# Optimization experiments

Hardware: AMD Instinct MI355X
Metric: run time of the kernel (lower is better)

Reference implementation:

```python
import jax, jax.numpy as jnp
import numpy as np

CHEB_K = 2  # chebyshev polynomial order (support_ks = [I, A] for cheb_k=2)


def _fc(x, w1, b1, w2, b2, w3, b3):
    # FC module: Linear -> sigmoid -> Linear -> sigmoid -> Linear
    h = jax.nn.sigmoid(x @ w1 + b1)
    h = jax.nn.sigmoid(h @ w2 + b2)
    return h @ w3 + b3


def _preprocess(adj):
    # adj: [B,N,N]; add self-loops then row-normalize
    adj = adj + jnp.eye(adj.shape[-1], dtype=adj.dtype)
    return adj / adj.sum(-1, keepdims=True)


def _gcn(x, adjs, ne, wpool, bpool):
    # x: [B,N,C], adjs: list of [B,N,N], ne: [N,E]
    # wpool: [E, 2*CHEB_K, C, O], bpool: [E, O]
    mats = []
    for A in adjs:
        ks = [jnp.broadcast_to(jnp.eye(A.shape[-1], dtype=A.dtype), A.shape), A]
        for _ in range(2, CHEB_K):
            ks.append(2.0 * jnp.matmul(A, ks[-1]) - ks[-2])
        mats.extend(ks)
    # [B,N,K,C] with K = 2*CHEB_K
    x_g = jnp.stack([jnp.einsum('bnm,bmc->bnc', S, x) for S in mats], axis=2)
    weights = jnp.einsum('nd,dkio->nkio', ne, wpool)  # [N,K,C,O]
    bias = ne @ bpool  # [N,O]
    return jnp.einsum('bnki,nkio->bno', x_g, weights) + bias


def _forward(x, state, ne0, ne1, ne2, fc1_w1, fc1_b1, fc1_w2, fc1_b2, fc1_w3, fc1_b3,
             fc2_w1, fc2_b1, fc2_w2, fc2_b2, fc2_w3, fc2_b3, gate_w, gate_b, upd_w, upd_b):
    hid = upd_w.shape[-1]
    ins = jnp.concatenate([x, state], axis=-1)  # [B,N,dim_in+hid]
    f1 = _fc(ins, fc1_w1, fc1_b1, fc1_w2, fc1_b2, fc1_w3, fc1_b3)  # [B,N,TD]
    f2 = _fc(ins, fc2_w1, fc2_b1, fc2_w2, fc2_b2, fc2_w3, fc2_b3)
    nv1 = jnp.tanh(ne0[:, None, :] * f1)  # einsum 'bd,bnd->bnd' == broadcast mul
    nv2 = jnp.tanh(ne1[:, None, :] * f2)
    adj = jnp.einsum('bnd,bmd->bnm', nv1, nv2) - jnp.einsum('bnd,bmd->bnm', nv2, nv1)
    adj1 = _preprocess(jax.nn.relu(adj))
    adj2 = _preprocess(jax.nn.relu(-jnp.swapaxes(adj, -2, -1)))
    z_r = jax.nn.sigmoid(_gcn(ins, [adj1, adj2], ne2, gate_w, gate_b))
    z, r = z_r[..., :hid], z_r[..., hid:]
    cand = jnp.concatenate([x, z * state], axis=-1)
    hc = jnp.tanh(_gcn(cand, [adj1, adj2], ne2, upd_w, upd_b))
    return r * state + (1.0 - r) * hc


def setup_inputs():
    B, N, DIN, DOUT, ED, TD = 32, 1024, 2, 64, 10, 32
    HG, MID = 16, 2  # hyperGNN_dim, middle_dim hardcoded in FC
    CIN = DIN + DOUT
    K2 = 2 * CHEB_K
    ks = jax.random.split(jax.random.key(0), 16)
    rn = lambda i, shape, s=1.0: jax.random.normal(ks[i], shape, dtype=jnp.float32) * s
    return {
        'x': rn(0, (B, N, DIN)),
        'state': rn(1, (B, N, DOUT)),
        'ne0': rn(2, (B, TD)),
        'ne1': rn(3, (B, TD)),
        'ne2': rn(4, (N, ED), 0.1),
        'fc1_w1': rn(5, (CIN, HG), 0.1), 'fc1_b1': jnp.zeros((HG,), jnp.float32),
        'fc1_w2': rn(6, (HG, MID), 0.1), 'fc1_b2': jnp.zeros((MID,), jnp.float32),
        'fc1_w3': rn(7, (MID, TD), 0.1), 'fc1_b3': jnp.zeros((TD,), jnp.float32),
        'fc2_w1': rn(8, (CIN, HG), 0.1), 'fc2_b1': jnp.zeros((HG,), jnp.float32),
        'fc2_w2': rn(9, (HG, MID), 0.1), 'fc2_b2': jnp.zeros((MID,), jnp.float32),
        'fc2_w3': rn(10, (MID, TD), 0.1), 'fc2_b3': jnp.zeros((TD,), jnp.float32),
        'gate_w': rn(11, (ED, K2, CIN, 2 * DOUT), 0.1),
        'gate_b': rn(12, (ED, 2 * DOUT), 0.1),
        'upd_w': rn(13, (ED, K2, CIN, DOUT), 0.1),
        'upd_b': rn(14, (ED, DOUT), 0.1),
    }


def reference(x, state, ne0, ne1, ne2, fc1_w1, fc1_b1, fc1_w2, fc1_b2, fc1_w3, fc1_b3,
              fc2_w1, fc2_b1, fc2_w2, fc2_b2, fc2_w3, fc2_b3, gate_w, gate_b, upd_w, upd_b):
    return _forward(x, state, ne0, ne1, ne2, fc1_w1, fc1_b1, fc1_w2, fc1_b2, fc1_w3, fc1_b3,
                    fc2_w1, fc2_b1, fc2_w2, fc2_b2, fc2_w3, fc2_b3, gate_w, gate_b, upd_w, upd_b)
```

## Files before the change

### kernel.cpp

```cpp
#include <hip/hip_runtime.h>
#include <math.h>

#define BB   32
#define NN   1024
#define DIN  2
#define DOUT 64
#define CIN  66
#define TD   32
#define ED   10
#define OG   128
#define OU   64
#define KP   160
#define XTR  80
#define PS   88

typedef __bf16 bf16x8 __attribute__((ext_vector_type(8)));
typedef float  f32x4  __attribute__((ext_vector_type(4)));
typedef short  s16x8  __attribute__((ext_vector_type(8)));

__device__ __forceinline__ unsigned short f2b(float f) {
    __bf16 h = (__bf16)f;
    return *(unsigned short*)&h;
}

__global__ __launch_bounds__(256) void k_pre(
    const float* __restrict__ x, const float* __restrict__ state,
    const float* __restrict__ ne0, const float* __restrict__ ne1,
    const float* __restrict__ ne2,
    const float* __restrict__ w11, const float* __restrict__ b11,
    const float* __restrict__ w12, const float* __restrict__ b12,
    const float* __restrict__ w13, const float* __restrict__ b13,
    const float* __restrict__ w21, const float* __restrict__ b21,
    const float* __restrict__ w22, const float* __restrict__ b22,
    const float* __restrict__ w23, const float* __restrict__ b23,
    const float* __restrict__ gate_w, const float* __restrict__ gate_b,
    const float* __restrict__ upd_w, const float* __restrict__ upd_b,
    unsigned short* __restrict__ nv1b, unsigned short* __restrict__ nv2b,
    unsigned short* __restrict__ XT0, unsigned short* __restrict__ XT1,
    unsigned short* __restrict__ BcTg, unsigned short* __restrict__ BcTu,
    float* __restrict__ biasG, float* __restrict__ biasU)
{
    __shared__ float sw[2408];
    __shared__ unsigned short st[68*72];
    int blk = blockIdx.x;
    int t = threadIdx.x;

    if (blk < 128) {
        const int oW1 = 0, oB1 = 1056, oW2 = 1072, oB2 = 1104, oW3 = 1108, oB3 = 1172, F2 = 1204;
        for (int i = t; i < 1056; i += 256) { sw[oW1+i] = w11[i]; sw[F2+oW1+i] = w21[i]; }
        if (t < 16) { sw[oB1+t] = b11[t]; sw[F2+oB1+t] = b21[t]; }
        if (t < 32) { sw[oW2+t] = w12[t]; sw[F2+oW2+t] = w22[t]; }
        if (t < 2)  { sw[oB2+t] = b12[t]; sw[F2+oB2+t] = b22[t]; }
        if (t < 64) { sw[oW3+t] = w13[t]; sw[F2+oW3+t] = w23[t]; }
        if (t >= 64 && t < 96) { sw[oB3+t-64] = b13[t-64]; sw[F2+oB3+t-64] = b23[t-64]; }
        __syncthreads();

        int p = blk*256 + t;
        int b = p >> 10;

        float h1a[16], h1b[16];
        #pragma unroll
        for (int j = 0; j < 16; ++j) { h1a[j] = sw[oB1+j]; h1b[j] = sw[F2+oB1+j]; }
        for (int i = 0; i < CIN; ++i) {
            float v = (i < DIN) ? x[(size_t)p*DIN + i] : state[(size_t)p*DOUT + (i-DIN)];
            #pragma unroll
            for (int jq = 0; jq < 4; ++jq) {
                float4 wa = *(const float4*)&sw[oW1 + i*16 + jq*4];
                float4 wb = *(const float4*)&sw[F2 + oW1 + i*16 + jq*4];
                h1a[jq*4+0] += v*wa.x; h1a[jq*4+1] += v*wa.y;
                h1a[jq*4+2] += v*wa.z; h1a[jq*4+3] += v*wa.w;
                h1b[jq*4+0] += v*wb.x; h1b[jq*4+1] += v*wb.y;
                h1b[jq*4+2] += v*wb.z; h1b[jq*4+3] += v*wb.w;
            }
        }
        #pragma unroll
        for (int j = 0; j < 16; ++j) {
            h1a[j] = 1.f/(1.f + __expf(-h1a[j]));
            h1b[j] = 1.f/(1.f + __expf(-h1b[j]));
        }
        float h2a0 = sw[oB2+0], h2a1 = sw[oB2+1];
        float h2b0 = sw[F2+oB2+0], h2b1 = sw[F2+oB2+1];
        #pragma unroll
        for (int i = 0; i < 16; ++i) {
            h2a0 += h1a[i]*sw[oW2 + i*2 + 0];
            h2a1 += h1a[i]*sw[oW2 + i*2 + 1];
            h2b0 += h1b[i]*sw[F2+oW2 + i*2 + 0];
            h2b1 += h1b[i]*sw[F2+oW2 + i*2 + 1];
        }
        h2a0 = 1.f/(1.f + __expf(-h2a0)); h2a1 = 1.f/(1.f + __expf(-h2a1));
        h2b0 = 1.f/(1.f + __expf(-h2b0)); h2b1 = 1.f/(1.f + __expf(-h2b1));

        const float* pn0 = ne0 + b*TD;
        const float* pn1 = ne1 + b*TD;
        #pragma unroll
        for (int jq = 0; jq < 8; ++jq) {
            float4 ba  = *(const float4*)&sw[oB3 + jq*4];
            float4 wa0 = *(const float4*)&sw[oW3 + jq*4];
            float4 wa1 = *(const float4*)&sw[oW3 + 32 + jq*4];
            float4 bb2 = *(const float4*)&sw[F2+oB3 + jq*4];
            float4 wb0 = *(const float4*)&sw[F2+oW3 + jq*4];
            float4 wb1 = *(const float4*)&sw[F2+oW3 + 32 + jq*4];
            float4 n0 = *(const float4*)&pn0[jq*4];
            float4 n1 = *(const float4*)&pn1[jq*4];
            ushort4 u1, u2;
            u1.x = f2b(tanhf(n0.x*(ba.x + h2a0*wa0.x + h2a1*wa1.x)));
            u1.y = f2b(tanhf(n0.y*(ba.y + h2a0*wa0.y + h2a1*wa1.y)));
            u1.z = f2b(tanhf(n0.z*(ba.z + h2a0*wa0.z + h2a1*wa1.z)));
            u1.w = f2b(tanhf(n0.w*(ba.w + h2a0*wa0.w + h2a1*wa1.w)));
            u2.x = f2b(tanhf(n1.x*(bb2.x + h2b0*wb0.x + h2b1*wb1.x)));
            u2.y = f2b(tanhf(n1.y*(bb2.y + h2b0*wb0.y + h2b1*wb1.y)));
            u2.z = f2b(tanhf(n1.z*(bb2.z + h2b0*wb0.z + h2b1*wb1.z)));
            u2.w = f2b(tanhf(n1.w*(bb2.w + h2b0*wb0.w + h2b1*wb1.w)));
            *(ushort4*)&nv1b[(size_t)p*TD + jq*4] = u1;
            *(ushort4*)&nv2b[(size_t)p*TD + jq*4] = u2;
        }
    } else if (blk < 640) {
        int idx = blk - 128;
        int b = idx >> 4, m0 = (idx & 15)*64;
        for (int i = t; i < 1024; i += 256) {
            int m = i >> 4, cq = i & 15;
            size_t base = (size_t)b*NN + m0 + m;
            float4 v = *(const float4*)&state[base*DOUT + cq*4];
            st[(2 + cq*4 + 0)*72 + m] = f2b(v.x);
            st[(2 + cq*4 + 1)*72 + m] = f2b(v.y);
            st[(2 + cq*4 + 2)*72 + m] = f2b(v.z);
            st[(2 + cq*4 + 3)*72 + m] = f2b(v.w);
        }
        if (t < 128) {
            int m = t >> 1, c = t & 1;
            st[c*72 + m] = f2b(x[((size_t)b*NN + m0 + m)*DIN + c]);
        }
        __syncthreads();
        const unsigned int ONE2 = 0x3F803F80u;
        for (int i = t; i < XTR*8; i += 256) {
            int c = i >> 3, ch = i & 7;
            uint4 v;
            if (c < 66)      v = *(const uint4*)&st[c*72 + ch*8];
            else if (c == 66) v = make_uint4(ONE2, ONE2, ONE2, ONE2);
            else              v = make_uint4(0, 0, 0, 0);
            *(uint4*)&XT0[((size_t)b*XTR + c)*NN + m0 + ch*8] = v;
            if (c < 2 || c >= 66)
                *(uint4*)&XT1[((size_t)b*XTR + c)*NN + m0 + ch*8] = v;
        }
    } else if (blk < 1840) {
        int tid = (blk - 640)*256 + t;
        int c = tid / KP, k = tid - c*KP;
        const float* pool; int O, cc; unsigned short* dst;
        if (c < 1280) { pool = gate_w; O = OG; cc = c;        dst = BcTg; }
        else          { pool = upd_w;  O = OU; cc = c - 1280; dst = BcTu; }
        int d = cc / O, o = cc - d*O;
        float v = 0.f;
        if (k < 132) {
            int kp = (k < 66) ? 0 : 1;
            int i  = (k < 66) ? k : k - 66;
            v = pool[(size_t)((d*4 + kp)*CIN + i)*O + o]
              + pool[(size_t)((d*4 + kp + 2)*CIN + i)*O + o];
        }
        dst[(size_t)cc*KP + k] = f2b(v);
    } else {
        int i = (blk - 1840)*256 + t;
        int n = i / 192, j = i - n*192;
        float v = 0.f;
        if (j < 128) {
            #pragma unroll
            for (int d = 0; d < ED; ++d) v += ne2[(size_t)n*ED + d]*gate_b[d*OG + j];
            biasG[(size_t)n*OG + j] = v;
        } else {
            int o = j - 128;
            #pragma unroll
            for (int d = 0; d < ED; ++d) v += ne2[(size_t)n*ED + d]*upd_b[d*OU + o];
            biasU[(size_t)n*OU + o] = v;
        }
    }
}

__global__ __launch_bounds__(512) void k_aapply(
    const unsigned short* __restrict__ nv1b, const unsigned short* __restrict__ nv2b,
    const unsigned short* __restrict__ XTg, unsigned short* __restrict__ A)
{
    __shared__ unsigned short s_nv1r[64*40], s_nv2r[64*40];
    __shared__ unsigned short s_nv1c[64*40], s_nv2c[64*40];
    __shared__ unsigned short s_p[64*PS];
    __shared__ unsigned short s_xt[80*72];
    __shared__ float s_rs[64];

    int t = threadIdx.x;
    int id = blockIdx.x;
    int b = id & 31, rbase = (id >> 5)*64;
    int w = t >> 6, lane = t & 63, lq = lane >> 4, ln = lane & 15;
    int g = w >> 1, sub = w & 1;

    {
        int arr = t >> 8, j = t & 255;
        int node = j >> 2, ch = j & 3;
        const unsigned short* src = (arr ? nv2b : nv1b)
            + ((size_t)b*NN + rbase + node)*TD + ch*8;
        unsigned short* dst = (arr ? s_nv2r : s_nv1r) + node*40 + ch*8;
        *(uint4*)dst = *(const uint4*)src;
    }
    __syncthreads();

    bf16x8 a1 = *(const bf16x8*)&s_nv1r[(16*g + ln)*40 + lq*8];
    s16x8 a2s = *(const s16x8*)&s_nv2r[(16*g + ln)*40 + lq*8];
    const s16x8 sgn = {(short)0x8000,(short)0x8000,(short)0x8000,(short)0x8000,
                       (short)0x8000,(short)0x8000,(short)0x8000,(short)0x8000};
    a2s ^= sgn;
    bf16x8 a2n = (bf16x8)a2s;

    f32x4 acc[3];
    #pragma unroll
    for (int i = 0; i < 3; ++i) acc[i] = (f32x4){0.f,0.f,0.f,0.f};
    const f32x4 zero4 = {0.f,0.f,0.f,0.f};

    for (int mb = 0; mb < NN; mb += 64) {
        __syncthreads();
        {
            int arr = t >> 8, j = t & 255;
            int node = j >> 2, ch = j & 3;
            const unsigned short* src = (arr ? nv2b : nv1b)
                + ((size_t)b*NN + mb + node)*TD + ch*8;
            unsigned short* dst = (arr ? s_nv2c : s_nv1c) + node*40 + ch*8;
            *(uint4*)dst = *(const uint4*)src;
        }
        for (int i = t; i < 640; i += 512) {
            int c = i >> 3, ch = i & 7;
            *(uint4*)&s_xt[c*72 + ch*8] =
                *(const uint4*)&XTg[((size_t)b*XTR + c)*NN + mb + ch*8];
        }
        __syncthreads();

        #pragma unroll
        for (int jj = 0; jj < 2; ++jj) {
            int j0 = (sub*2 + jj)*16;
            bf16x8 b2 = *(const bf16x8*)&s_nv2c[(j0 + ln)*40 + lq*8];
            bf16x8 b1 = *(const bf16x8*)&s_nv1c[(j0 + ln)*40 + lq*8];
            f32x4 s = __builtin_amdgcn_mfma_f32_16x16x32_bf16(a1,  b2, zero4, 0, 0, 0);
            s       = __builtin_amdgcn_mfma_f32_16x16x32_bf16(a2n, b1, s,     0, 0, 0);
            #pragma unroll
            for (int r = 0; r < 4; ++r) {
                float p = fmaxf(s[r], 0.f);
                *(__bf16*)&s_p[(16*g + lq*4 + r)*PS + j0 + ln] = (__bf16)p;
            }
        }
        __syncthreads();

        bf16x8 pa0 = *(const bf16x8*)&s_p[(16*g + ln)*PS +      lq*8];
        bf16x8 pa1 = *(const bf16x8*)&s_p[(16*g + ln)*PS + 32 + lq*8];
        if (sub == 0) {
            #pragma unroll
            for (int k = 0; k < 3; ++k) {
                int n0 = k*16;
                bf16x8 xb0 = *(const bf16x8*)&s_xt[(n0 + ln)*72 +      lq*8];
                bf16x8 xb1 = *(const bf16x8*)&s_xt[(n0 + ln)*72 + 32 + lq*8];
                acc[k] = __builtin_amdgcn_mfma_f32_16x16x32_bf16(pa0, xb0, acc[k], 0, 0, 0);
                acc[k] = __builtin_amdgcn_mfma_f32_16x16x32_bf16(pa1, xb1, acc[k], 0, 0, 0);
            }
        } else {
            #pragma unroll
            for (int k = 0; k < 2; ++k) {
                int n0 = (3 + k)*16;
                bf16x8 xb0 = *(const bf16x8*)&s_xt[(n0 + ln)*72 +      lq*8];
                bf16x8 xb1 = *(const bf16x8*)&s_xt[(n0 + ln)*72 + 32 + lq*8];
                acc[k] = __builtin_amdgcn_mfma_f32_16x16x32_bf16(pa0, xb0, acc[k], 0, 0, 0);
                acc[k] = __builtin_amdgcn_mfma_f32_16x16x32_bf16(pa1, xb1, acc[k], 0, 0, 0);
            }
        }
    }

    if (sub == 1 && ln == 2) {
        #pragma unroll
        for (int r = 0; r < 4; ++r) s_rs[16*g + lq*4 + r] = acc[1][r];
    }
    __syncthreads();
    float rinv[4];
    #pragma unroll
    for (int r = 0; r < 4; ++r) rinv[r] = 1.0f / (1.0f + s_rs[16*g + lq*4 + r]);

    int kmax = sub ? 2 : 3;
    for (int k = 0; k < kmax; ++k) {
        int c = (sub ? (3 + k) : k)*16 + ln;
        if (c < CIN) {
            #pragma unroll
            for (int r = 0; r < 4; ++r) {
                int gr = rbase + 16*g + lq*4 + r;
                size_t rowG = (size_t)b*NN + gr;
                unsigned short xu = XTg[((size_t)b*XTR + c)*NN + gr];
                float xr = (float)(*(const __bf16*)&xu);
                A[rowG*KP + c]      = xu;
                A[rowG*KP + 66 + c] = f2b((acc[k][r] + xr) * rinv[r]);
            }
        }
    }
    for (int i = t; i < 64*28; i += 512) {
        int rr = i / 28, cc = 132 + (i - 28*(i/28));
        A[((size_t)b*NN + rbase + rr)*KP + cc] = 0;
    }
}

template<int O, int MODE>
__global__ __launch_bounds__(256) void k_gemm(
    const unsigned short* __restrict__ A, const unsigned short* __restrict__ BcT,
    const float* __restrict__ ne2, const float* __restrict__ biasP,
    const float* __restrict__ state, unsigned short* __restrict__ XT1,
    float* __restrict__ rbuf, float* __restrict__ out)
{
    __shared__ unsigned short s_b[80*168];

    int t = threadIdx.x;
    int w = t >> 6, lane = t & 63, lq = lane >> 4, ln = lane & 15;
    int o0 = blockIdx.y*16;
    int rowBlock = blockIdx.x*128;
    int rowW = rowBlock + w*32;

    f32x4 acc[2][2][5];
    #pragma unroll
    for (int h = 0; h < 2; ++h)
        #pragma unroll
        for (int f = 0; f < 2; ++f)
            #pragma unroll
            for (int c = 0; c < 5; ++c) acc[h][f][c] = (f32x4){0.f,0.f,0.f,0.f};

    #pragma unroll
    for (int h = 0; h < 2; ++h) {
        if (h) __syncthreads();
        for (int i = t; i < 1600; i += 256) {
            int cc = i / 20, kc = i - cc*20;
            int d = h*5 + (cc >> 4), oo = cc & 15;
            *(uint4*)&s_b[cc*168 + kc*8] =
                *(const uint4*)&BcT[(size_t)(d*O + o0 + oo)*KP + kc*8];
        }
        __syncthreads();

        #pragma unroll
        for (int kc = 0; kc < 5; ++kc) {
            bf16x8 af0 = *(const bf16x8*)&A[(size_t)(rowW      + ln)*KP + kc*32 + lq*8];
            bf16x8 af1 = *(const bf16x8*)&A[(size_t)(rowW + 16 + ln)*KP + kc*32 + lq*8];
            #pragma unroll
            for (int ct = 0; ct < 5; ++ct) {
                bf16x8 bf = *(const bf16x8*)&s_b[(ct*16 + ln)*168 + kc*32 + lq*8];
                acc[h][0][ct] = __builtin_amdgcn_mfma_f32_16x16x32_bf16(af0, bf, acc[h][0][ct], 0, 0, 0);
                acc[h][1][ct] = __builtin_amdgcn_mfma_f32_16x16x32_bf16(af1, bf, acc[h][1][ct], 0, 0, 0);
            }
        }
    }

    int o = o0 + ln;
    #pragma unroll
    for (int f = 0; f < 2; ++f) {
        #pragma unroll
        for (int r = 0; r < 4; ++r) {
            int row_l = w*32 + 16*f + lq*4 + r;
            size_t rowG = (size_t)rowBlock + row_l;
            int n = (int)(rowG & (NN - 1));
            int bb = (int)(rowG >> 10);
            const float* nep = &ne2[(size_t)n*ED];
            float val = biasP[(size_t)n*O + o];
            #pragma unroll
            for (int d = 0; d < 5; ++d) val += nep[d]     * acc[0][f][d][r];
            #pragma unroll
            for (int d = 0; d < 5; ++d) val += nep[5 + d] * acc[1][f][d][r];
            if (MODE == 0) {
                float sv = 1.f/(1.f + __expf(-val));
                if (o0 < 64) {
                    float zst = sv * state[rowG*DOUT + o];
                    XT1[((size_t)bb*XTR + 2 + o)*NN + n] = f2b(zst);
                } else {
                    rbuf[rowG*DOUT + (o - 64)] = sv;
                }
            } else {
                float hc = tanhf(val);
                float rg = rbuf[rowG*DOUT + o];
                float st = state[rowG*DOUT + o];
                out[rowG*DOUT + o] = rg*st + (1.f - rg)*hc;
            }
        }
    }
}

extern "C" void kernel_launch(void* const* d_in, const int* in_sizes, int n_in,
                              void* d_out, int out_size, void* d_ws, size_t ws_size,
                              hipStream_t stream)
{
    const float* x      = (const float*)d_in[0];
    const float* state  = (const float*)d_in[1];
    const float* ne0    = (const float*)d_in[2];
    const float* ne1    = (const float*)d_in[3];
    const float* ne2    = (const float*)d_in[4];
    const float* f1w1   = (const float*)d_in[5];
    const float* f1b1   = (const float*)d_in[6];
    const float* f1w2   = (const float*)d_in[7];
    const float* f1b2   = (const float*)d_in[8];
    const float* f1w3   = (const float*)d_in[9];
    const float* f1b3   = (const float*)d_in[10];
    const float* f2w1   = (const float*)d_in[11];
    const float* f2b1   = (const float*)d_in[12];
    const float* f2w2   = (const float*)d_in[13];
    const float* f2b2   = (const float*)d_in[14];
    const float* f2w3   = (const float*)d_in[15];
    const float* f2b3   = (const float*)d_in[16];
    const float* gate_w = (const float*)d_in[17];
    const float* gate_b = (const float*)d_in[18];
    const float* upd_w  = (const float*)d_in[19];
    const float* upd_b  = (const float*)d_in[20];

    unsigned short* nv1b = (unsigned short*)d_ws;
    unsigned short* nv2b = nv1b + (size_t)BB*NN*TD;
    unsigned short* XT0  = nv2b + (size_t)BB*NN*TD;
    unsigned short* XT1  = XT0  + (size_t)BB*XTR*NN;
    unsigned short* A    = XT1  + (size_t)BB*XTR*NN;
    unsigned short* BcTg = A    + (size_t)BB*NN*KP;
    unsigned short* BcTu = BcTg + (size_t)1280*KP;
    float* biasG = (float*)(BcTu + (size_t)640*KP);
    float* biasU = biasG + (size_t)NN*OG;
    float* rbuf  = biasU + (size_t)NN*OU;
    float* out   = (float*)d_out;

    k_pre<<<dim3(2608), 256, 0, stream>>>(x, state, ne0, ne1, ne2,
        f1w1, f1b1, f1w2, f1b2, f1w3, f1b3,
        f2w1, f2b1, f2w2, f2b2, f2w3, f2b3,
        gate_w, gate_b, upd_w, upd_b,
        nv1b, nv2b, XT0, XT1, BcTg, BcTu, biasG, biasU);

    k_aapply<<<dim3(512), 512, 0, stream>>>(nv1b, nv2b, XT0, A);

    k_gemm<OG,0><<<dim3(BB*NN/128, 8), 256, 0, stream>>>(A, BcTg, ne2, biasG,
                                                         state, XT1, rbuf, nullptr);

    k_aapply<<<dim3(512), 512, 0, stream>>>(nv1b, nv2b, XT1, A);

    k_gemm<OU,1><<<dim3(BB*NN/128, 4), 256, 0, stream>>>(A, BcTu, ne2, biasU,
                                                         state, nullptr, rbuf, out);
}
```

Baseline: 238.3 us.

## Rework adjacency-apply kernel to keep P tile in registers via lane permutes

The k_aapply kernel no longer stages nv1/nv2/XT tiles and the relu'd score tile P in shared memory with block barriers. Each wave now computes a 16-row strip by loading operands directly from global memory and transposing the score MFMA (swapped operands). It converts results to the MFMA A-operand layout with v_cvt_pk_bf16 plus permlane32/16 swaps, then accumulates all 5 output column tiles itself. This removes LDS traffic and __syncthreads per iteration at the cost of halving block size (256 threads), more redundant global/L2 reads, and reliance on gfx950-specific permlane instructions.

```diff
diff --git a/kernel.cpp b/kernel.cpp
--- a/kernel.cpp
+++ b/kernel.cpp
@@ -12,7 +12,6 @@
 #define OU   64
 #define KP   160
 #define XTR  80
-#define PS   88
 
 typedef __bf16 bf16x8 __attribute__((ext_vector_type(8)));
 typedef float  f32x4  __attribute__((ext_vector_type(4)));
@@ -21,6 +20,18 @@
 __device__ __forceinline__ unsigned short f2b(float f) {
     __bf16 h = (__bf16)f;
     return *(unsigned short*)&h;
+}
+
+__device__ __forceinline__ unsigned int cvt_pk_bf16(float lo, float hi) {
+    unsigned int r;
+    asm("v_cvt_pk_bf16_f32 %0, %1, %2" : "=v"(r) : "v"(lo), "v"(hi));
+    return r;
+}
+__device__ __forceinline__ void perm32swap(unsigned int& a, unsigned int& b) {
+    asm("v_permlane32_swap_b32 %0, %1" : "+v"(a), "+v"(b));
+}
+__device__ __forceinline__ void perm16swap(unsigned int& a, unsigned int& b) {
+    asm("v_permlane16_swap_b32 %0, %1" : "+v"(a), "+v"(b));
 }
 
 __global__ __launch_bounds__(256) void k_pre(
@@ -174,115 +185,79 @@
     }
 }
 
-__global__ __launch_bounds__(512) void k_aapply(
+__global__ __launch_bounds__(256) void k_aapply(
     const unsigned short* __restrict__ nv1b, const unsigned short* __restrict__ nv2b,
     const unsigned short* __restrict__ XTg, unsigned short* __restrict__ A)
 {
-    __shared__ unsigned short s_nv1r[64*40], s_nv2r[64*40];
-    __shared__ unsigned short s_nv1c[64*40], s_nv2c[64*40];
-    __shared__ unsigned short s_p[64*PS];
-    __shared__ unsigned short s_xt[80*72];
-    __shared__ float s_rs[64];
-
     int t = threadIdx.x;
     int id = blockIdx.x;
     int b = id & 31, rbase = (id >> 5)*64;
     int w = t >> 6, lane = t & 63, lq = lane >> 4, ln = lane & 15;
-    int g = w >> 1, sub = w & 1;
-
-    {
-        int arr = t >> 8, j = t & 255;
-        int node = j >> 2, ch = j & 3;
-        const unsigned short* src = (arr ? nv2b : nv1b)
-            + ((size_t)b*NN + rbase + node)*TD + ch*8;
-        unsigned short* dst = (arr ? s_nv2r : s_nv1r) + node*40 + ch*8;
-        *(uint4*)dst = *(const uint4*)src;
-    }
-    __syncthreads();
-
-    bf16x8 a1 = *(const bf16x8*)&s_nv1r[(16*g + ln)*40 + lq*8];
-    s16x8 a2s = *(const s16x8*)&s_nv2r[(16*g + ln)*40 + lq*8];
+
+    bf16x8 a1 = *(const bf16x8*)&nv1b[((size_t)b*NN + rbase + 16*w + ln)*TD + lq*8];
+    s16x8 a2s = *(const s16x8*)&nv2b[((size_t)b*NN + rbase + 16*w + ln)*TD + lq*8];
     const s16x8 sgn = {(short)0x8000,(short)0x8000,(short)0x8000,(short)0x8000,
                        (short)0x8000,(short)0x8000,(short)0x8000,(short)0x8000};
     a2s ^= sgn;
     bf16x8 a2n = (bf16x8)a2s;
 
-    f32x4 acc[3];
-    #pragma unroll
-    for (int i = 0; i < 3; ++i) acc[i] = (f32x4){0.f,0.f,0.f,0.f};
+    const unsigned short* nc1 = nv1b + ((size_t)b*NN + ln)*TD + lq*8;
+    const unsigned short* nc2 = nv2b + ((size_t)b*NN + ln)*TD + lq*8;
+    const unsigned short* xtp = XTg + ((size_t)b*XTR + ln)*NN + lq*8;
+
+    f32x4 acc[5];
+    #pragma unroll
+    for (int k = 0; k < 5; ++k) acc[k] = (f32x4){0.f,0.f,0.f,0.f};
     const f32x4 zero4 = {0.f,0.f,0.f,0.f};
 
+    union U8 { unsigned int u[4]; bf16x8 v; };
+
     for (int mb = 0; mb < NN; mb += 64) {
-        __syncthreads();
-        {
-            int arr = t >> 8, j = t & 255;
-            int node = j >> 2, ch = j & 3;
-            const unsigned short* src = (arr ? nv2b : nv1b)
-                + ((size_t)b*NN + mb + node)*TD + ch*8;
-            unsigned short* dst = (arr ? s_nv2c : s_nv1c) + node*40 + ch*8;
-            *(uint4*)dst = *(const uint4*)src;
-        }
-        for (int i = t; i < 640; i += 512) {
-            int c = i >> 3, ch = i & 7;
-            *(uint4*)&s_xt[c*72 + ch*8] =
-                *(const uint4*)&XTg[((size_t)b*XTR + c)*NN + mb + ch*8];
-        }
-        __syncthreads();
-
-        #pragma unroll
-        for (int jj = 0; jj < 2; ++jj) {
-            int j0 = (sub*2 + jj)*16;
-            bf16x8 b2 = *(const bf16x8*)&s_nv2c[(j0 + ln)*40 + lq*8];
-            bf16x8 b1 = *(const bf16x8*)&s_nv1c[(j0 + ln)*40 + lq*8];
-            f32x4 s = __builtin_amdgcn_mfma_f32_16x16x32_bf16(a1,  b2, zero4, 0, 0, 0);
-            s       = __builtin_amdgcn_mfma_f32_16x16x32_bf16(a2n, b1, s,     0, 0, 0);
+        unsigned int u[4][2];
+        #pragma unroll
+        for (int jj = 0; jj < 4; ++jj) {
+            size_t off = (size_t)(mb + jj*16)*TD;
+            bf16x8 b2 = *(const bf16x8*)(nc2 + off);
+            bf16x8 b1 = *(const bf16x8*)(nc1 + off);
+            f32x4 s = __builtin_amdgcn_mfma_f32_16x16x32_bf16(b2, a1,  zero4, 0, 0, 0);
+            s       = __builtin_amdgcn_mfma_f32_16x16x32_bf16(b1, a2n, s,     0, 0, 0);
+            u[jj][0] = cvt_pk_bf16(fmaxf(s[0], 0.f), fmaxf(s[1], 0.f));
+            u[jj][1] = cvt_pk_bf16(fmaxf(s[2], 0.f), fmaxf(s[3], 0.f));
+        }
+
+        unsigned int w00 = u[0][0], w20 = u[1][0]; perm32swap(w00, w20); perm16swap(w00, w20);
+        unsigned int w01 = u[0][1], w21 = u[1][1]; perm32swap(w01, w21); perm16swap(w01, w21);
+        unsigned int x00 = u[2][0], x20 = u[3][0]; perm32swap(x00, x20); perm16swap(x00, x20);
+        unsigned int x01 = u[2][1], x21 = u[3][1]; perm32swap(x01, x21); perm16swap(x01, x21);
+        U8 p0, p1;
+        p0.u[0] = w00; p0.u[1] = w01; p0.u[2] = w20; p0.u[3] = w21;
+        p1.u[0] = x00; p1.u[1] = x01; p1.u[2] = x20; p1.u[3] = x21;
+        bf16x8 pa0 = p0.v, pa1 = p1.v;
+
+        #pragma unroll
+        for (int k = 0; k < 5; ++k) {
+            const unsigned short* xp = xtp + (size_t)(k*16)*NN + mb;
+            bf16x8 xb0 = *(const bf16x8*)xp;
+            bf16x8 xb1 = *(const bf16x8*)(xp + 32);
+            acc[k] = __builtin_amdgcn_mfma_f32_16x16x32_bf16(pa0, xb0, acc[k], 0, 0, 0);
+            acc[k] = __builtin_amdgcn_mfma_f32_16x16x32_bf16(pa1, xb1, acc[k], 0, 0, 0);
+        }
+    }
+
+    float rinv[4];
+    #pragma unroll
+    for (int r = 0; r < 4; ++r) {
+        float rs = __shfl(acc[4][r], (lane & 48) | 2, 64);
+        rinv[r] = 1.0f / (1.0f + rs);
+    }
+
+    #pragma unroll
+    for (int k = 0; k < 5; ++k) {
+        int c = k*16 + ln;
+        if (c < CIN) {
             #pragma unroll
             for (int r = 0; r < 4; ++r) {
-                float p = fmaxf(s[r], 0.f);
-                *(__bf16*)&s_p[(16*g + lq*4 + r)*PS + j0 + ln] = (__bf16)p;
-            }
-        }
-        __syncthreads();
-
-        bf16x8 pa0 = *(const bf16x8*)&s_p[(16*g + ln)*PS +      lq*8];
-        bf16x8 pa1 = *(const bf16x8*)&s_p[(16*g + ln)*PS + 32 + lq*8];
-        if (sub == 0) {
-            #pragma unroll
-            for (int k = 0; k < 3; ++k) {
-                int n0 = k*16;
-                bf16x8 xb0 = *(const bf16x8*)&s_xt[(n0 + ln)*72 +      lq*8];
-                bf16x8 xb1 = *(const bf16x8*)&s_xt[(n0 + ln)*72 + 32 + lq*8];
-                acc[k] = __builtin_amdgcn_mfma_f32_16x16x32_bf16(pa0, xb0, acc[k], 0, 0, 0);
-                acc[k] = __builtin_amdgcn_mfma_f32_16x16x32_bf16(pa1, xb1, acc[k], 0, 0, 0);
-            }
-        } else {
-            #pragma unroll
-            for (int k = 0; k < 2; ++k) {
-                int n0 = (3 + k)*16;
-                bf16x8 xb0 = *(const bf16x8*)&s_xt[(n0 + ln)*72 +      lq*8];
-                bf16x8 xb1 = *(const bf16x8*)&s_xt[(n0 + ln)*72 + 32 + lq*8];
-                acc[k] = __builtin_amdgcn_mfma_f32_16x16x32_bf16(pa0, xb0, acc[k], 0, 0, 0);
-                acc[k] = __builtin_amdgcn_mfma_f32_16x16x32_bf16(pa1, xb1, acc[k], 0, 0, 0);
-            }
-        }
-    }
-
-    if (sub == 1 && ln == 2) {
-        #pragma unroll
-        for (int r = 0; r < 4; ++r) s_rs[16*g + lq*4 + r] = acc[1][r];
-    }
-    __syncthreads();
-    float rinv[4];
-    #pragma unroll
-    for (int r = 0; r < 4; ++r) rinv[r] = 1.0f / (1.0f + s_rs[16*g + lq*4 + r]);
-
-    int kmax = sub ? 2 : 3;
-    for (int k = 0; k < kmax; ++k) {
-        int c = (sub ? (3 + k) : k)*16 + ln;
-        if (c < CIN) {
-            #pragma unroll
-            for (int r = 0; r < 4; ++r) {
-                int gr = rbase + 16*g + lq*4 + r;
+                int gr = rbase + 16*w + lq*4 + r;
                 size_t rowG = (size_t)b*NN + gr;
                 unsigned short xu = XTg[((size_t)b*XTR + c)*NN + gr];
                 float xr = (float)(*(const __bf16*)&xu);
@@ -291,7 +266,7 @@
             }
         }
     }
-    for (int i = t; i < 64*28; i += 512) {
+    for (int i = t; i < 64*28; i += 256) {
         int rr = i / 28, cc = 132 + (i - 28*(i/28));
         A[((size_t)b*NN + rbase + rr)*KP + cc] = 0;
     }
@@ -421,12 +396,12 @@
         gate_w, gate_b, upd_w, upd_b,
         nv1b, nv2b, XT0, XT1, BcTg, BcTu, biasG, biasU);
 
-    k_aapply<<<dim3(512), 512, 0, stream>>>(nv1b, nv2b, XT0, A);
+    k_aapply<<<dim3(512), 256, 0, stream>>>(nv1b, nv2b, XT0, A);
 
     k_gemm<OG,0><<<dim3(BB*NN/128, 8), 256, 0, stream>>>(A, BcTg, ne2, biasG,
                                                          state, XT1, rbuf, nullptr);
 
-    k_aapply<<<dim3(512), 512, 0, stream>>>(nv1b, nv2b, XT1, A);
+    k_aapply<<<dim3(512), 256, 0, stream>>>(nv1b, nv2b, XT1, A);
 
     k_gemm<OU,1><<<dim3(BB*NN/128, 4), 256, 0, stream>>>(A, BcTu, ne2, biasU,
                                                          state, nullptr, rbuf, out);
```

New measurement: 287.3 us. +20.6%, slower.
